# Kernel tuning notes

Hardware: AMD Instinct MI355X
Metric: run time of the kernel (lower is better)

Reference implementation:

```python
import jax, jax.numpy as jnp
import numpy as np

GX = GY = GZ = 128
VOXEL_DIM = 28  # 1 density + 27 SH coefficients (9 per RGB channel)
NUM_RAYS = 8192
NUM_SAMPLES = 128


def sh_basis(theta, phi):
    """Degree-2 SH basis in the coefficient order used by harmonic():
    [Y_0_0, Y_m1_1, Y_0_1, Y_1_1, Y_m2_2, Y_m1_2, Y_0_2, Y_1_2, Y_2_2]."""
    y00 = 0.5 * jnp.sqrt(1.0 / jnp.pi)
    h3 = 0.5 * jnp.sqrt(3.0 / jnp.pi)
    q5 = 0.25 * jnp.sqrt(5.0 / jnp.pi)
    h15 = 0.5 * jnp.sqrt(15.0 / jnp.pi)
    q15 = 0.25 * jnp.sqrt(15.0 / jnp.pi)
    st, ct = jnp.sin(theta), jnp.cos(theta)
    sp, cp = jnp.sin(phi), jnp.cos(phi)
    return jnp.stack([
        y00 * jnp.ones_like(theta),          # Y_0_0
        h3 * st * sp,                        # Y_m1_1
        h3 * ct,                             # Y_0_1
        h3 * st * cp,                        # Y_1_1
        h15 * st * cp * st * sp,             # Y_m2_2
        h15 * st * sp * ct,                  # Y_m1_2
        q5 * (3.0 * ct * ct - 1.0),          # Y_0_2
        h15 * st * cp * ct,                  # Y_1_2
        q15 * ((st * cp) ** 2 - (st * sp) ** 2),  # Y_2_2
    ])


def trilinear(grid, pos):
    """grid: [GX,GY,GZ,D]; pos: [R,S,3] -> [R,S,D] interpolated features."""
    p0 = jnp.floor(pos).astype(jnp.int32)
    fr = pos - p0.astype(pos.dtype)
    x0, y0, z0 = p0[..., 0], p0[..., 1], p0[..., 2]
    xd, yd, zd = fr[..., 0:1], fr[..., 1:2], fr[..., 2:3]
    c000 = grid[x0, y0, z0]
    c001 = grid[x0, y0, z0 + 1]
    c010 = grid[x0, y0 + 1, z0]
    c011 = grid[x0, y0 + 1, z0 + 1]
    c100 = grid[x0 + 1, y0, z0]
    c101 = grid[x0 + 1, y0, z0 + 1]
    c110 = grid[x0 + 1, y0 + 1, z0]
    c111 = grid[x0 + 1, y0 + 1, z0 + 1]
    c00 = c000 * (1 - xd) + c100 * xd
    c01 = c001 * (1 - xd) + c101 * xd
    c10 = c010 * (1 - xd) + c110 * xd
    c11 = c011 * (1 - xd) + c111 * xd
    c0 = c00 * (1 - yd) + c10 * yd
    c1 = c01 * (1 - yd) + c11 * yd
    return c0 * (1 - zd) + c1 * zd


def setup_inputs() -> dict:
    key = jax.random.key(0)
    k1, k2, k3, k4 = jax.random.split(key, 4)
    voxel_grid = jax.random.uniform(k1, (GX, GY, GZ, VOXEL_DIM), dtype=jnp.float32)
    # sample positions inside [0, G-2] so the +1 corner stays in bounds
    sample_positions = jax.random.uniform(
        k2, (NUM_RAYS, NUM_SAMPLES, 3), dtype=jnp.float32) * (GX - 2)
    sample_distances = jax.random.uniform(
        k3, (NUM_RAYS, NUM_SAMPLES), dtype=jnp.float32) * 0.1
    viewing_angle = jax.random.uniform(k4, (2,), dtype=jnp.float32) * np.pi
    return {
        "voxel_grid": voxel_grid,
        "sample_positions": sample_positions,
        "sample_distances": sample_distances,
        "viewing_angle": viewing_angle,
    }


def reference(voxel_grid, sample_positions, sample_distances, viewing_angle):
    R, S = sample_distances.shape
    feats = trilinear(voxel_grid, sample_positions)          # [R,S,28]
    sigma = feats[..., 0]                                     # [R,S]
    sh_coeffs = feats[..., 1:].reshape(R, S, 3, 9)            # [R,S,3,9]
    basis = sh_basis(viewing_angle[0], viewing_angle[1])      # [9]
    rgb = jnp.einsum('rsck,k->rsc', sh_coeffs, basis)         # [R,S,3]
    tau = sigma * sample_distances                            # [R,S]
    att = jnp.exp(-tau)
    # faithful to channel_opacity_z: transmittance is the CUMULATIVE SUM of
    # exp(-sigma_j * d_j) over j = 0..k (inclusive of current sample)
    transmittance = jnp.cumsum(att, axis=1)
    alpha = 1.0 - att
    weights = transmittance * alpha                           # [R,S]
    return jnp.sum(weights[..., None] * rgb, axis=1)          # [R,3]
```

## Files before the change

### kernel.cpp

```cpp
#include <hip/hip_runtime.h>
#include <hip/hip_fp16.h>
#include <math.h>

#define GXD 128
#define GYD 128
#define GZD 128
#define VD 28
#define VDP 32
#define NRAYS 8192
#define NSAMP 128

__global__ __launch_bounds__(256) void convert_grid(
    const float* __restrict__ g, __half* __restrict__ h)
{
    const unsigned t = blockIdx.x * 256u + threadIdx.x;
    const unsigned o = t << 1;
    const unsigned v = o >> 5;
    const unsigned k = o & 31;
    __half2 out;
    if (k < VD) {
        const float2 f = *(const float2*)(g + v * VD + k);
        out = __floats2half2_rn(f.x, f.y);
    } else {
        out = __floats2half2_rn(0.0f, 0.0f);
    }
    *(__half2*)(h + o) = out;
}

__global__ __launch_bounds__(1024) void plenoxel_fused16(
    const __half* __restrict__ hg,
    const float* __restrict__ pos,
    const float* __restrict__ dist,
    const float* __restrict__ ang,
    float* __restrict__ out)
{
    __shared__ float4 srgb[NSAMP];

    const int ray  = blockIdx.x;
    const int tid  = threadIdx.x;
    const int s    = tid >> 3;
    const int subl = tid & 7;
    const int dx   = (subl >> 2) & 1;
    const int dy   = (subl >> 1) & 1;
    const int zh   = subl & 1;

    const float theta = ang[0], phi = ang[1];
    float st, ct, sp, cp;
    sincosf(theta, &st, &ct);
    sincosf(phi,   &sp, &cp);
    float basis[9];
    basis[0] = 0.28209479177387814f;
    basis[1] = 0.4886025119029199f * st * sp;
    basis[2] = 0.4886025119029199f * ct;
    basis[3] = 0.4886025119029199f * st * cp;
    basis[4] = 1.0925484305920792f * st * cp * st * sp;
    basis[5] = 1.0925484305920792f * st * sp * ct;
    basis[6] = 0.31539156525252005f * (3.0f * ct * ct - 1.0f);
    basis[7] = 1.0925484305920792f * st * cp * ct;
    basis[8] = 0.5462742152960396f * ((st * cp) * (st * cp) - (st * sp) * (st * sp));

    const int sidx = ray * NSAMP + s;
    const float px = pos[sidx * 3 + 0];
    const float py = pos[sidx * 3 + 1];
    const float pz = pos[sidx * 3 + 2];
    const int ix = (int)floorf(px);
    const int iy = (int)floorf(py);
    const int iz = (int)floorf(pz);
    const float fx = px - (float)ix;
    const float fy = py - (float)iy;
    const float fz = pz - (float)iz;

    const float w = (dx ? fx : 1.0f - fx) *
                    (dy ? fy : 1.0f - fy) *
                    (zh ? fz : 1.0f - fz);

    const int base = (((ix + dx) * GYD + (iy + dy)) * GZD + (iz + zh)) * VDP;
    const float4* __restrict__ q = (const float4*)(hg + base);

    float4 raw[4];
    raw[0] = q[0]; raw[1] = q[1]; raw[2] = q[2]; raw[3] = q[3];
    const __half* f = (const __half*)raw;

    float sig = __half2float(f[0]);
    float r = 0.0f, g = 0.0f, b = 0.0f;
    #pragma unroll
    for (int k = 0; k < 9; ++k) {
        r += basis[k] * __half2float(f[1 + k]);
        g += basis[k] * __half2float(f[10 + k]);
        b += basis[k] * __half2float(f[19 + k]);
    }
    float psig = w * sig;
    float pr = w * r, pg = w * g, pb = w * b;

    #pragma unroll
    for (int off = 1; off < 8; off <<= 1) {
        psig += __shfl_xor(psig, off, 64);
        pr   += __shfl_xor(pr,   off, 64);
        pg   += __shfl_xor(pg,   off, 64);
        pb   += __shfl_xor(pb,   off, 64);
    }
    if (subl == 0) srgb[s] = make_float4(psig, pr, pg, pb);
    __syncthreads();

    if (tid < 64) {
        const int lane = tid;
        const float4 a0 = srgb[lane];
        const float4 a1 = srgb[lane + 64];
        const float d0 = dist[ray * NSAMP + lane];
        const float d1 = dist[ray * NSAMP + lane + 64];
        const float att0 = expf(-a0.x * d0);
        const float att1 = expf(-a1.x * d1);

        float scan_lo = att0;
        #pragma unroll
        for (int off = 1; off < 64; off <<= 1) {
            const float v = __shfl_up(scan_lo, off, 64);
            if (lane >= off) scan_lo += v;
        }
        const float total_lo = __shfl(scan_lo, 63, 64);

        float scan_hi = att1;
        #pragma unroll
        for (int off = 1; off < 64; off <<= 1) {
            const float v = __shfl_up(scan_hi, off, 64);
            if (lane >= off) scan_hi += v;
        }
        const float w_lo = scan_lo * (1.0f - att0);
        const float w_hi = (total_lo + scan_hi) * (1.0f - att1);

        float o0 = w_lo * a0.y + w_hi * a1.y;
        float o1 = w_lo * a0.z + w_hi * a1.z;
        float o2 = w_lo * a0.w + w_hi * a1.w;

        #pragma unroll
        for (int off = 32; off > 0; off >>= 1) {
            o0 += __shfl_xor(o0, off, 64);
            o1 += __shfl_xor(o1, off, 64);
            o2 += __shfl_xor(o2, off, 64);
        }
        if (lane == 0) {
            out[ray * 3 + 0] = o0;
            out[ray * 3 + 1] = o1;
            out[ray * 3 + 2] = o2;
        }
    }
}

__global__ __launch_bounds__(1024) void plenoxel_fused32(
    const float* __restrict__ grid,
    const float* __restrict__ pos,
    const float* __restrict__ dist,
    const float* __restrict__ ang,
    float* __restrict__ out)
{
    __shared__ float4 srgb[NSAMP];
    const int ray  = blockIdx.x;
    const int tid  = threadIdx.x;
    const int s    = tid >> 3;
    const int subl = tid & 7;
    const int dx   = (subl >> 2) & 1;
    const int dy   = (subl >> 1) & 1;
    const int zh   = subl & 1;

    const float theta = ang[0], phi = ang[1];
    float st, ct, sp, cp;
    sincosf(theta, &st, &ct);
    sincosf(phi,   &sp, &cp);
    float basis[9];
    basis[0] = 0.28209479177387814f;
    basis[1] = 0.4886025119029199f * st * sp;
    basis[2] = 0.4886025119029199f * ct;
    basis[3] = 0.4886025119029199f * st * cp;
    basis[4] = 1.0925484305920792f * st * cp * st * sp;
    basis[5] = 1.0925484305920792f * st * sp * ct;
    basis[6] = 0.31539156525252005f * (3.0f * ct * ct - 1.0f);
    basis[7] = 1.0925484305920792f * st * cp * ct;
    basis[8] = 0.5462742152960396f * ((st * cp) * (st * cp) - (st * sp) * (st * sp));

    const int sidx = ray * NSAMP + s;
    const float px = pos[sidx * 3 + 0];
    const float py = pos[sidx * 3 + 1];
    const float pz = pos[sidx * 3 + 2];
    const int ix = (int)floorf(px);
    const int iy = (int)floorf(py);
    const int iz = (int)floorf(pz);
    const float fx = px - (float)ix;
    const float fy = py - (float)iy;
    const float fz = pz - (float)iz;

    const float w = (dx ? fx : 1.0f - fx) *
                    (dy ? fy : 1.0f - fy) *
                    (zh ? fz : 1.0f - fz);

    const int base = (((ix + dx) * GYD + (iy + dy)) * GZD + (iz + zh)) * VD;
    const float4* __restrict__ q = (const float4*)(grid + base);
    float f[28];
    #pragma unroll
    for (int i = 0; i < 7; ++i)
        ((float4*)f)[i] = q[i];

    float psig = w * f[0];
    float pr = 0.0f, pg = 0.0f, pb = 0.0f;
    #pragma unroll
    for (int k = 0; k < 9; ++k) {
        pr += basis[k] * f[1 + k];
        pg += basis[k] * f[10 + k];
        pb += basis[k] * f[19 + k];
    }
    pr *= w; pg *= w; pb *= w;

    #pragma unroll
    for (int off = 1; off < 8; off <<= 1) {
        psig += __shfl_xor(psig, off, 64);
        pr   += __shfl_xor(pr,   off, 64);
        pg   += __shfl_xor(pg,   off, 64);
        pb   += __shfl_xor(pb,   off, 64);
    }
    if (subl == 0) srgb[s] = make_float4(psig, pr, pg, pb);
    __syncthreads();

    if (tid < 64) {
        const int lane = tid;
        const float4 a0 = srgb[lane];
        const float4 a1 = srgb[lane + 64];
        const float d0 = dist[ray * NSAMP + lane];
        const float d1 = dist[ray * NSAMP + lane + 64];
        const float att0 = expf(-a0.x * d0);
        const float att1 = expf(-a1.x * d1);

        float scan_lo = att0;
        #pragma unroll
        for (int off = 1; off < 64; off <<= 1) {
            const float v = __shfl_up(scan_lo, off, 64);
            if (lane >= off) scan_lo += v;
        }
        const float total_lo = __shfl(scan_lo, 63, 64);
        float scan_hi = att1;
        #pragma unroll
        for (int off = 1; off < 64; off <<= 1) {
            const float v = __shfl_up(scan_hi, off, 64);
            if (lane >= off) scan_hi += v;
        }
        const float w_lo = scan_lo * (1.0f - att0);
        const float w_hi = (total_lo + scan_hi) * (1.0f - att1);

        float o0 = w_lo * a0.y + w_hi * a1.y;
        float o1 = w_lo * a0.z + w_hi * a1.z;
        float o2 = w_lo * a0.w + w_hi * a1.w;
        #pragma unroll
        for (int off = 32; off > 0; off >>= 1) {
            o0 += __shfl_xor(o0, off, 64);
            o1 += __shfl_xor(o1, off, 64);
            o2 += __shfl_xor(o2, off, 64);
        }
        if (lane == 0) {
            out[ray * 3 + 0] = o0;
            out[ray * 3 + 1] = o1;
            out[ray * 3 + 2] = o2;
        }
    }
}

extern "C" void kernel_launch(void* const* d_in, const int* in_sizes, int n_in,
                              void* d_out, int out_size, void* d_ws, size_t ws_size,
                              hipStream_t stream) {
    const float* grid = (const float*)d_in[0];
    const float* pos  = (const float*)d_in[1];
    const float* dist = (const float*)d_in[2];
    const float* ang  = (const float*)d_in[3];
    float* out = (float*)d_out;

    const size_t need = (size_t)GXD * GYD * GZD * VDP * sizeof(__half);
    if (ws_size >= need) {
        __half* hg = (__half*)d_ws;
        const unsigned n_half2 = (unsigned)((size_t)GXD * GYD * GZD * VDP / 2);
        convert_grid<<<n_half2 / 256, 256, 0, stream>>>(grid, hg);
        plenoxel_fused16<<<NRAYS, 1024, 0, stream>>>(hg, pos, dist, ang, out);
    } else {
        plenoxel_fused32<<<NRAYS, 1024, 0, stream>>>(grid, pos, dist, ang, out);
    }
}
```

Before: 446.2 us.

## Bin samples by spatial bucket to improve grid gather locality

Replaces the fp16 grid conversion plus per-ray fused kernel with a pipeline that hashes each sample into an 8^3-voxel spatial bucket, builds a histogram and scan, scatters sample ids into bucket order, shades samples bucket by bucket straight from the fp32 grid, and then composites per ray in a separate pass. The goal is cache locality for the random trilinear gathers and dropping the per-call full-grid conversion. In exchange it adds six launches, global atomics, an unordered per-bucket id scatter and a 16 MB intermediate results buffer. Each bucket holds about 256 samples but is processed by only 256 threads, so parallelism per block is limited.

```diff
diff --git a/kernel.cpp b/kernel.cpp
--- a/kernel.cpp
+++ b/kernel.cpp
@@ -1,44 +1,107 @@
 #include <hip/hip_runtime.h>
-#include <hip/hip_fp16.h>
 #include <math.h>
 
 #define GXD 128
 #define GYD 128
 #define GZD 128
 #define VD 28
-#define VDP 32
 #define NRAYS 8192
 #define NSAMP 128
-
-__global__ __launch_bounds__(256) void convert_grid(
-    const float* __restrict__ g, __half* __restrict__ h)
-{
-    const unsigned t = blockIdx.x * 256u + threadIdx.x;
-    const unsigned o = t << 1;
-    const unsigned v = o >> 5;
-    const unsigned k = o & 31;
-    __half2 out;
-    if (k < VD) {
-        const float2 f = *(const float2*)(g + v * VD + k);
-        out = __floats2half2_rn(f.x, f.y);
-    } else {
-        out = __floats2half2_rn(0.0f, 0.0f);
-    }
-    *(__half2*)(h + o) = out;
-}
-
-__global__ __launch_bounds__(1024) void plenoxel_fused16(
-    const __half* __restrict__ hg,
+#define NTOT (NRAYS * NSAMP)
+#define NBUCKET 4096
+
+
+__global__ __launch_bounds__(256) void zero_hist(unsigned* __restrict__ hist) {
+    const int i = blockIdx.x * 256 + threadIdx.x;
+    if (i < NBUCKET) hist[i] = 0;
+}
+
+__global__ __launch_bounds__(256) void hist_keys(
+    const float* __restrict__ pos, unsigned* __restrict__ keys,
+    unsigned* __restrict__ hist)
+{
+    __shared__ unsigned lh[NBUCKET];
+    for (int i = threadIdx.x; i < NBUCKET; i += 256) lh[i] = 0;
+    __syncthreads();
+    for (int s = blockIdx.x * 256 + threadIdx.x; s < NTOT; s += gridDim.x * 256) {
+        const float px = pos[3 * s + 0];
+        const float py = pos[3 * s + 1];
+        const float pz = pos[3 * s + 2];
+        const int ix = (int)floorf(px);
+        const int iy = (int)floorf(py);
+        const int iz = (int)floorf(pz);
+        const unsigned key = ((unsigned)(ix >> 3) << 8) |
+                             ((unsigned)(iy >> 3) << 4) |
+                              (unsigned)(iz >> 3);
+        keys[s] = key;
+        atomicAdd(&lh[key], 1u);
+    }
+    __syncthreads();
+    for (int i = threadIdx.x; i < NBUCKET; i += 256) {
+        const unsigned c = lh[i];
+        if (c) atomicAdd(&hist[i], c);
+    }
+}
+
+__global__ __launch_bounds__(1024) void scan_buckets(
+    const unsigned* __restrict__ hist, unsigned* __restrict__ offsets,
+    unsigned* __restrict__ cursors)
+{
+    __shared__ unsigned wsum[16];
+    const int t = threadIdx.x;
+    const int lane = t & 63;
+    const int wv = t >> 6;
+    unsigned v[4];
+    unsigned s = 0;
+    #pragma unroll
+    for (int i = 0; i < 4; ++i) { v[i] = hist[4 * t + i]; s += v[i]; }
+    unsigned sc = s;
+    #pragma unroll
+    for (int off = 1; off < 64; off <<= 1) {
+        const unsigned u = __shfl_up(sc, off, 64);
+        if (lane >= off) sc += u;
+    }
+    if (lane == 63) wsum[wv] = sc;
+    __syncthreads();
+    if (t == 0) {
+        unsigned acc = 0;
+        for (int i = 0; i < 16; ++i) { const unsigned x = wsum[i]; wsum[i] = acc; acc += x; }
+    }
+    __syncthreads();
+    unsigned excl = wsum[wv] + (sc - s);
+    #pragma unroll
+    for (int i = 0; i < 4; ++i) {
+        offsets[4 * t + i] = excl;
+        cursors[4 * t + i] = excl;
+        excl += v[i];
+    }
+    if (t == 1023) offsets[NBUCKET] = excl;
+}
+
+__global__ __launch_bounds__(256) void scatter_ids(
+    const unsigned* __restrict__ keys, unsigned* __restrict__ cursors,
+    unsigned* __restrict__ ids)
+{
+    for (int s = blockIdx.x * 256 + threadIdx.x; s < NTOT; s += gridDim.x * 256) {
+        const unsigned k = keys[s];
+        const unsigned idx = atomicAdd(&cursors[k], 1u);
+        ids[idx] = s;
+    }
+}
+
+__global__ __launch_bounds__(256) void shade(
+    const float* __restrict__ grid,
     const float* __restrict__ pos,
-    const float* __restrict__ dist,
+    const unsigned* __restrict__ offsets,
+    const unsigned* __restrict__ ids,
     const float* __restrict__ ang,
-    float* __restrict__ out)
-{
-    __shared__ float4 srgb[NSAMP];
-
-    const int ray  = blockIdx.x;
+    float4* __restrict__ results)
+{
+    const unsigned b = blockIdx.x;
+    const unsigned begin = offsets[b];
+    const unsigned end   = offsets[b + 1];
+
     const int tid  = threadIdx.x;
-    const int s    = tid >> 3;
     const int subl = tid & 7;
     const int dx   = (subl >> 2) & 1;
     const int dy   = (subl >> 1) & 1;
@@ -59,90 +122,100 @@
     basis[7] = 1.0925484305920792f * st * cp * ct;
     basis[8] = 0.5462742152960396f * ((st * cp) * (st * cp) - (st * sp) * (st * sp));
 
-    const int sidx = ray * NSAMP + s;
-    const float px = pos[sidx * 3 + 0];
-    const float py = pos[sidx * 3 + 1];
-    const float pz = pos[sidx * 3 + 2];
-    const int ix = (int)floorf(px);
-    const int iy = (int)floorf(py);
-    const int iz = (int)floorf(pz);
-    const float fx = px - (float)ix;
-    const float fy = py - (float)iy;
-    const float fz = pz - (float)iz;
-
-    const float w = (dx ? fx : 1.0f - fx) *
-                    (dy ? fy : 1.0f - fy) *
-                    (zh ? fz : 1.0f - fz);
-
-    const int base = (((ix + dx) * GYD + (iy + dy)) * GZD + (iz + zh)) * VDP;
-    const float4* __restrict__ q = (const float4*)(hg + base);
-
-    float4 raw[4];
-    raw[0] = q[0]; raw[1] = q[1]; raw[2] = q[2]; raw[3] = q[3];
-    const __half* f = (const __half*)raw;
-
-    float sig = __half2float(f[0]);
-    float r = 0.0f, g = 0.0f, b = 0.0f;
-    #pragma unroll
-    for (int k = 0; k < 9; ++k) {
-        r += basis[k] * __half2float(f[1 + k]);
-        g += basis[k] * __half2float(f[10 + k]);
-        b += basis[k] * __half2float(f[19 + k]);
-    }
-    float psig = w * sig;
-    float pr = w * r, pg = w * g, pb = w * b;
-
-    #pragma unroll
-    for (int off = 1; off < 8; off <<= 1) {
-        psig += __shfl_xor(psig, off, 64);
-        pr   += __shfl_xor(pr,   off, 64);
-        pg   += __shfl_xor(pg,   off, 64);
-        pb   += __shfl_xor(pb,   off, 64);
-    }
-    if (subl == 0) srgb[s] = make_float4(psig, pr, pg, pb);
-    __syncthreads();
-
-    if (tid < 64) {
-        const int lane = tid;
-        const float4 a0 = srgb[lane];
-        const float4 a1 = srgb[lane + 64];
-        const float d0 = dist[ray * NSAMP + lane];
-        const float d1 = dist[ray * NSAMP + lane + 64];
-        const float att0 = expf(-a0.x * d0);
-        const float att1 = expf(-a1.x * d1);
-
-        float scan_lo = att0;
-        #pragma unroll
-        for (int off = 1; off < 64; off <<= 1) {
-            const float v = __shfl_up(scan_lo, off, 64);
-            if (lane >= off) scan_lo += v;
-        }
-        const float total_lo = __shfl(scan_lo, 63, 64);
-
-        float scan_hi = att1;
-        #pragma unroll
-        for (int off = 1; off < 64; off <<= 1) {
-            const float v = __shfl_up(scan_hi, off, 64);
-            if (lane >= off) scan_hi += v;
-        }
-        const float w_lo = scan_lo * (1.0f - att0);
-        const float w_hi = (total_lo + scan_hi) * (1.0f - att1);
-
-        float o0 = w_lo * a0.y + w_hi * a1.y;
-        float o1 = w_lo * a0.z + w_hi * a1.z;
-        float o2 = w_lo * a0.w + w_hi * a1.w;
-
-        #pragma unroll
-        for (int off = 32; off > 0; off >>= 1) {
-            o0 += __shfl_xor(o0, off, 64);
-            o1 += __shfl_xor(o1, off, 64);
-            o2 += __shfl_xor(o2, off, 64);
-        }
-        if (lane == 0) {
-            out[ray * 3 + 0] = o0;
-            out[ray * 3 + 1] = o1;
-            out[ray * 3 + 2] = o2;
-        }
+    for (unsigned j0 = begin; j0 < end; j0 += 32) {
+        const unsigned j = j0 + (unsigned)(tid >> 3);
+        if (j < end) {
+            const unsigned s = ids[j];
+            const float px = pos[3 * s + 0];
+            const float py = pos[3 * s + 1];
+            const float pz = pos[3 * s + 2];
+            const int ix = (int)floorf(px);
+            const int iy = (int)floorf(py);
+            const int iz = (int)floorf(pz);
+            const float fx = px - (float)ix;
+            const float fy = py - (float)iy;
+            const float fz = pz - (float)iz;
+
+            const float w = (dx ? fx : 1.0f - fx) *
+                            (dy ? fy : 1.0f - fy) *
+                            (zh ? fz : 1.0f - fz);
+
+            const int base = (((ix + dx) * GYD + (iy + dy)) * GZD + (iz + zh)) * VD;
+            const float4* __restrict__ q = (const float4*)(grid + base);
+            float f[28];
+            #pragma unroll
+            for (int i = 0; i < 7; ++i)
+                ((float4*)f)[i] = q[i];
+
+            float psig = w * f[0];
+            float pr = 0.0f, pg = 0.0f, pb = 0.0f;
+            #pragma unroll
+            for (int k = 0; k < 9; ++k) {
+                pr += basis[k] * f[1 + k];
+                pg += basis[k] * f[10 + k];
+                pb += basis[k] * f[19 + k];
+            }
+            pr *= w; pg *= w; pb *= w;
+
+            #pragma unroll
+            for (int off = 1; off < 8; off <<= 1) {
+                psig += __shfl_xor(psig, off, 64);
+                pr   += __shfl_xor(pr,   off, 64);
+                pg   += __shfl_xor(pg,   off, 64);
+                pb   += __shfl_xor(pb,   off, 64);
+            }
+            if (subl == 0) results[s] = make_float4(psig, pr, pg, pb);
+        }
+    }
+}
+
+__global__ __launch_bounds__(256) void composite(
+    const float4* __restrict__ results,
+    const float* __restrict__ dist,
+    float* __restrict__ out)
+{
+    const int wave = threadIdx.x >> 6;
+    const int lane = threadIdx.x & 63;
+    const int ray  = blockIdx.x * 4 + wave;
+
+    const float4 a0 = results[ray * NSAMP + lane];
+    const float4 a1 = results[ray * NSAMP + lane + 64];
+    const float d0 = dist[ray * NSAMP + lane];
+    const float d1 = dist[ray * NSAMP + lane + 64];
+    const float att0 = expf(-a0.x * d0);
+    const float att1 = expf(-a1.x * d1);
+
+    float scan_lo = att0;
+    #pragma unroll
+    for (int off = 1; off < 64; off <<= 1) {
+        const float v = __shfl_up(scan_lo, off, 64);
+        if (lane >= off) scan_lo += v;
+    }
+    const float total_lo = __shfl(scan_lo, 63, 64);
+
+    float scan_hi = att1;
+    #pragma unroll
+    for (int off = 1; off < 64; off <<= 1) {
+        const float v = __shfl_up(scan_hi, off, 64);
+        if (lane >= off) scan_hi += v;
+    }
+    const float w_lo = scan_lo * (1.0f - att0);
+    const float w_hi = (total_lo + scan_hi) * (1.0f - att1);
+
+    float o0 = w_lo * a0.y + w_hi * a1.y;
+    float o1 = w_lo * a0.z + w_hi * a1.z;
+    float o2 = w_lo * a0.w + w_hi * a1.w;
+
+    #pragma unroll
+    for (int off = 32; off > 0; off >>= 1) {
+        o0 += __shfl_xor(o0, off, 64);
+        o1 += __shfl_xor(o1, off, 64);
+        o2 += __shfl_xor(o2, off, 64);
+    }
+    if (lane == 0) {
+        out[ray * 3 + 0] = o0;
+        out[ray * 3 + 1] = o1;
+        out[ray * 3 + 2] = o2;
     }
 }
 
@@ -270,12 +343,22 @@
     const float* ang  = (const float*)d_in[3];
     float* out = (float*)d_out;
 
-    const size_t need = (size_t)GXD * GYD * GZD * VDP * sizeof(__half);
+    char* ws = (char*)d_ws;
+    unsigned* hist    = (unsigned*)(ws);
+    unsigned* offsets = (unsigned*)(ws + 32768);
+    unsigned* cursors = (unsigned*)(ws + 65536);
+    unsigned* keys    = (unsigned*)(ws + 131072);
+    unsigned* ids     = (unsigned*)(ws + 131072 + (size_t)NTOT * 4);
+    float4*   results = (float4*)  (ws + 131072 + (size_t)NTOT * 8);
+    const size_t need = 131072 + (size_t)NTOT * (4 + 4 + 16);
+
     if (ws_size >= need) {
-        __half* hg = (__half*)d_ws;
-        const unsigned n_half2 = (unsigned)((size_t)GXD * GYD * GZD * VDP / 2);
-        convert_grid<<<n_half2 / 256, 256, 0, stream>>>(grid, hg);
-        plenoxel_fused16<<<NRAYS, 1024, 0, stream>>>(hg, pos, dist, ang, out);
+        zero_hist<<<16, 256, 0, stream>>>(hist);
+        hist_keys<<<1024, 256, 0, stream>>>(pos, keys, hist);
+        scan_buckets<<<1, 1024, 0, stream>>>(hist, offsets, cursors);
+        scatter_ids<<<1024, 256, 0, stream>>>(keys, cursors, ids);
+        shade<<<NBUCKET, 256, 0, stream>>>(grid, pos, offsets, ids, ang, results);
+        composite<<<NRAYS / 4, 256, 0, stream>>>(results, dist, out);
     } else {
         plenoxel_fused32<<<NRAYS, 1024, 0, stream>>>(grid, pos, dist, ang, out);
     }
```

Result: slower. 633.0 us (+41.8%).
